# Performance work log

Hardware: AMD Instinct MI355X
Metric: run time of the kernel (lower is better)

The kernel has to match this reference:

```python
import jax, jax.numpy as jnp
import numpy as np

N_EMBED = 1024
EMBED_DIM = 256

def setup_inputs() -> dict:
    key = jax.random.key(0)
    k1, k2 = jax.random.split(key)
    hidden_states = jax.random.normal(k1, (64, 32, 32, EMBED_DIM), dtype=jnp.float32)
    emb_weights = jax.random.normal(k2, (N_EMBED, EMBED_DIM), dtype=jnp.float32)
    return {"hidden_states": hidden_states, "emb_weights": emb_weights}

def reference(hidden_states, emb_weights):
    # flatten (B,H,W,C) -> (N, C) with C == embed_dim
    z_flat = hidden_states.reshape((-1, EMBED_DIM))
    # squared distance: ||z||^2 + ||e||^2 - 2 z.e
    distance = (
        jnp.sum(z_flat ** 2, axis=1, keepdims=True)
        + jnp.sum(emb_weights ** 2, axis=1)
        - 2.0 * jnp.dot(z_flat, emb_weights.T)
    )  # (N, n_embed)
    min_encoding_indices = jnp.argmin(distance, axis=1)  # (N,)
    z_q = jnp.take(emb_weights, min_encoding_indices, axis=0).reshape(hidden_states.shape)
    min_encoding_indices = min_encoding_indices.reshape(hidden_states.shape[0], -1)
    return z_q, min_encoding_indices
```

## Files before the change

kernel.cpp:

```cpp
#include <hip/hip_runtime.h>

typedef _Float16 half8  __attribute__((ext_vector_type(8)));
typedef _Float16 half4  __attribute__((ext_vector_type(4)));
typedef float    float4v __attribute__((ext_vector_type(4)));
typedef float    float8v __attribute__((ext_vector_type(8)));

#define N_ROWS  65536
#define N_CODES 1024
#define DIM     256
#define BM      64
#define NBLKS   (N_ROWS / BM)

__global__ __launch_bounds__(64)
void vq_prep(const float* __restrict__ emb, float* __restrict__ e_norm,
             _Float16* __restrict__ e_frag, int* __restrict__ count) {
    const int c = blockIdx.x, lane = threadIdx.x;
    const int l15 = c & 15, nt = c >> 4;
    if (count && c == 0 && lane == 0) *count = 0;
    float4v v = ((const float4v*)(emb + (size_t)c * DIM))[lane];
    half4 h, l;
    float ss = 0.f;
    #pragma unroll
    for (int j = 0; j < 4; ++j) {
        float x = v[j];
        ss += x * x;
        _Float16 hh = (_Float16)x;
        h[j] = hh;
        l[j] = (_Float16)(x - (float)hh);
    }
    const int ks = lane >> 3, q = (lane >> 1) & 3, jb = (lane & 1) * 4;
    _Float16* p = e_frag + ((size_t)(nt * 8 + ks)) * 1024 + (q * 16 + l15) * 8 + jb;
    *(half4*)p = h;
    *(half4*)(p + 512) = l;
    #pragma unroll
    for (int m = 32; m >= 1; m >>= 1) ss += __shfl_xor(ss, m, 64);
    if (lane == 0) e_norm[c] = ss;
}

__global__ __launch_bounds__(256, 2)
void vq_screen(const float* __restrict__ z,
               const _Float16* __restrict__ e_frag,
               const float* __restrict__ e_norm,
               const float* __restrict__ emb,
               float* __restrict__ zq,
               float* __restrict__ idxf,
               int* __restrict__ count,
               int* __restrict__ list) {
    __shared__ _Float16 sA[32 * 512];
    __shared__ float    s_nrm[N_CODES];
    __shared__ float    s_znrm[BM];
    __shared__ float    s_red[4];
    __shared__ float4   s_best[BM][5];
    __shared__ int      s_idx[BM];

    const int t = threadIdx.x;
    const int w = t >> 6, lane = t & 63, quad = lane >> 4, l15 = lane & 15;
    const int rowblk = blockIdx.x * BM;

    float n0 = e_norm[t], n1 = e_norm[t + 256], n2 = e_norm[t + 512], n3 = e_norm[t + 768];
    s_nrm[t] = n0; s_nrm[t + 256] = n1; s_nrm[t + 512] = n2; s_nrm[t + 768] = n3;
    float mx = fmaxf(fmaxf(n0, n1), fmaxf(n2, n3));
    #pragma unroll
    for (int m = 1; m < 64; m <<= 1) mx = fmaxf(mx, __shfl_xor(mx, m, 64));
    if (lane == 0) s_red[w] = mx;

    float ss = 0.f;
    #pragma unroll
    for (int i = 0; i < 8; ++i) {
        const int row = w * 16 + l15;
        const int col = i * 32 + quad * 8;
        float8v v = *(const float8v*)(z + (size_t)(rowblk + row) * DIM + col);
        half8 h;
        #pragma unroll
        for (int j = 0; j < 8; ++j) {
            float x = v[j];
            ss += x * x;
            h[j] = (_Float16)x;
        }
        *(half8*)(sA + (size_t)(w * 8 + i) * 512 + lane * 8) = h;
    }
    ss += __shfl_xor(ss, 16, 64);
    ss += __shfl_xor(ss, 32, 64);
    if (quad == 0) s_znrm[w * 16 + l15] = ss;
    __syncthreads();

    for (int pass = 0; pass < 2; ++pass) {
        const int ntbase = w * 16 + pass * 8;
        float4v acc[4][8] = {};

        #pragma unroll
        for (int ks = 0; ks < 8; ++ks) {
            half8 bh[8];
            #pragma unroll
            for (int nt = 0; nt < 8; ++nt)
                bh[nt] = *(const half8*)(e_frag + ((size_t)((ntbase + nt) * 8 + ks)) * 1024 + lane * 8);
            __builtin_amdgcn_s_setprio(1);
            #pragma unroll
            for (int mt = 0; mt < 4; ++mt) {
                half8 ah = *(const half8*)(sA + (size_t)(mt * 8 + ks) * 512 + lane * 8);
                #pragma unroll
                for (int nt = 0; nt < 8; ++nt)
                    acc[mt][nt] = __builtin_amdgcn_mfma_f32_16x16x32_f16(ah, bh[nt], acc[mt][nt], 0, 0, 0);
            }
            __builtin_amdgcn_s_setprio(0);
        }

        float nrm[8]; int cg[8];
        #pragma unroll
        for (int nt = 0; nt < 8; ++nt) {
            cg[nt]  = (ntbase + nt) * 16 + l15;
            nrm[nt] = s_nrm[cg[nt]];
        }
        #pragma unroll
        for (int mt = 0; mt < 4; ++mt) {
            #pragma unroll
            for (int r = 0; r < 4; ++r) {
                float m1 = nrm[0] - 2.0f * acc[mt][0][r]; int i1 = cg[0];
                float m2 = 1e30f;
                #pragma unroll
                for (int nt = 1; nt < 8; ++nt) {
                    float s = nrm[nt] - 2.0f * acc[mt][nt][r];
                    if (s < m1) { m2 = m1; m1 = s; i1 = cg[nt]; }
                    else m2 = fminf(m2, s);
                }
                #pragma unroll
                for (int m = 1; m < 16; m <<= 1) {
                    float o1 = __shfl_xor(m1, m, 64);
                    int   oi = __shfl_xor(i1, m, 64);
                    float o2 = __shfl_xor(m2, m, 64);
                    if (o1 < m1 || (o1 == m1 && oi < i1)) {
                        m2 = fminf(m1, o2); m1 = o1; i1 = oi;
                    } else {
                        m2 = fminf(m2, o1);
                    }
                }
                if (l15 == 0) {
                    const int row = mt * 16 + quad * 4 + r;
                    if (pass == 0) {
                        float4 pr; pr.x = m1; pr.y = (float)i1; pr.z = m2; pr.w = 0.f;
                        s_best[row][w] = pr;
                    } else {
                        float4 pv = s_best[row][w];
                        float4 pr;
                        if (m1 < pv.x) { pr.x = m1; pr.y = (float)i1; pr.z = fminf(pv.x, m2); }
                        else           { pr.x = pv.x; pr.y = pv.y;     pr.z = fminf(pv.z, m1); }
                        pr.w = 0.f;
                        s_best[row][w] = pr;
                    }
                }
            }
        }
    }
    __syncthreads();

    if (t < BM) {
        float4 b0 = s_best[t][0];
        float m1 = b0.x, fi = b0.y, m2 = b0.z;
        #pragma unroll
        for (int s = 1; s < 4; ++s) {
            float4 bv = s_best[t][s];
            if (bv.x < m1 || (bv.x == m1 && bv.y < fi)) {
                m2 = fminf(m1, bv.z); m1 = bv.x; fi = bv.y;
            } else {
                m2 = fminf(m2, bv.x);
            }
        }
        s_idx[t] = (int)fi;
        idxf[rowblk + t] = fi;
        float emax = sqrtf(fmaxf(fmaxf(s_red[0], s_red[1]), fmaxf(s_red[2], s_red[3])));
        float T = 0.005f * sqrtf(s_znrm[t]) * emax + 0.05f;
        if (m2 - m1 <= T) {
            int pos = atomicAdd(count, 1);
            list[pos] = rowblk + t;
        }
    }
    __syncthreads();

    const float4v* emb4 = (const float4v*)emb;
    float4v* zq4 = (float4v*)zq;
    const int rr = t >> 2, cb = t & 3;
    const int code = s_idx[rr];
    #pragma unroll
    for (int i = 0; i < 16; ++i) {
        const int chunk = cb + i * 4;
        zq4[(size_t)(rowblk + rr) * 64 + chunk] = emb4[(size_t)code * 64 + chunk];
    }
}

__global__ __launch_bounds__(256, 2)
void vq_exact(const float* __restrict__ z,
              const _Float16* __restrict__ e_frag,
              const float* __restrict__ e_norm,
              const float* __restrict__ emb,
              float* __restrict__ zq,
              float* __restrict__ idxf,
              const int* __restrict__ count,
              const int* __restrict__ list) {
    const int cnt = *count;
    const int base = blockIdx.x * BM;
    if (base >= cnt) return;

    __shared__ _Float16 sA[32 * 2 * 512];
    __shared__ float    s_nrm[N_CODES];
    __shared__ float2   s_best[BM][5];
    __shared__ int      s_idx[BM];
    __shared__ int      s_rows[BM];

    const int t = threadIdx.x;
    const int w = t >> 6, lane = t & 63, quad = lane >> 4, l15 = lane & 15;

    if (t < BM) {
        int slot = base + t;
        s_rows[t] = list[slot < cnt ? slot : cnt - 1];
    }
    s_nrm[t]       = e_norm[t];
    s_nrm[t + 256] = e_norm[t + 256];
    s_nrm[t + 512] = e_norm[t + 512];
    s_nrm[t + 768] = e_norm[t + 768];
    __syncthreads();

    #pragma unroll
    for (int i = 0; i < 8; ++i) {
        const int row = w * 16 + l15;
        const int grow = s_rows[row];
        const int col = i * 32 + quad * 8;
        float8v v = *(const float8v*)(z + (size_t)grow * DIM + col);
        half8 h, lo;
        #pragma unroll
        for (int j = 0; j < 8; ++j) {
            float x = v[j];
            _Float16 hh = (_Float16)x;
            h[j] = hh;
            lo[j] = (_Float16)(x - (float)hh);
        }
        _Float16* p = sA + (size_t)((w * 8 + i) * 2) * 512 + lane * 8;
        *(half8*)p = h;
        *(half8*)(p + 512) = lo;
    }
    __syncthreads();

    for (int pass = 0; pass < 2; ++pass) {
        const int ntbase = w * 16 + pass * 8;
        float4v acc[4][8] = {};

        #pragma unroll
        for (int ks = 0; ks < 8; ++ks) {
            half8 bh[8], bl[8];
            #pragma unroll
            for (int nt = 0; nt < 8; ++nt) {
                const _Float16* bp = e_frag + ((size_t)((ntbase + nt) * 8 + ks)) * 1024 + lane * 8;
                bh[nt] = *(const half8*)bp;
                bl[nt] = *(const half8*)(bp + 512);
            }
            __builtin_amdgcn_s_setprio(1);
            #pragma unroll
            for (int mt = 0; mt < 4; ++mt) {
                const _Float16* ap = sA + (size_t)((mt * 8 + ks) * 2) * 512 + lane * 8;
                half8 ah = *(const half8*)ap;
                half8 al = *(const half8*)(ap + 512);
                #pragma unroll
                for (int nt = 0; nt < 8; ++nt)
                    acc[mt][nt] = __builtin_amdgcn_mfma_f32_16x16x32_f16(ah, bh[nt], acc[mt][nt], 0, 0, 0);
                #pragma unroll
                for (int nt = 0; nt < 8; ++nt)
                    acc[mt][nt] = __builtin_amdgcn_mfma_f32_16x16x32_f16(ah, bl[nt], acc[mt][nt], 0, 0, 0);
                #pragma unroll
                for (int nt = 0; nt < 8; ++nt)
                    acc[mt][nt] = __builtin_amdgcn_mfma_f32_16x16x32_f16(al, bh[nt], acc[mt][nt], 0, 0, 0);
            }
            __builtin_amdgcn_s_setprio(0);
        }

        float nrm[8]; int cg[8];
        #pragma unroll
        for (int nt = 0; nt < 8; ++nt) {
            cg[nt]  = (ntbase + nt) * 16 + l15;
            nrm[nt] = s_nrm[cg[nt]];
        }
        #pragma unroll
        for (int mt = 0; mt < 4; ++mt) {
            #pragma unroll
            for (int r = 0; r < 4; ++r) {
                float bs = nrm[0] - 2.0f * acc[mt][0][r]; int bi = cg[0];
                #pragma unroll
                for (int nt = 1; nt < 8; ++nt) {
                    float s = nrm[nt] - 2.0f * acc[mt][nt][r];
                    if (s < bs) { bs = s; bi = cg[nt]; }
                }
                #pragma unroll
                for (int m = 1; m < 16; m <<= 1) {
                    float s2 = __shfl_xor(bs, m, 64);
                    int   i2 = __shfl_xor(bi, m, 64);
                    if (s2 < bs || (s2 == bs && i2 < bi)) { bs = s2; bi = i2; }
                }
                if (l15 == 0) {
                    const int row = mt * 16 + quad * 4 + r;
                    if (pass == 0) {
                        float2 pr; pr.x = bs; pr.y = (float)bi;
                        s_best[row][w] = pr;
                    } else {
                        float2 pv = s_best[row][w];
                        if (bs < pv.x) {
                            float2 pr; pr.x = bs; pr.y = (float)bi;
                            s_best[row][w] = pr;
                        }
                    }
                }
            }
        }
    }
    __syncthreads();

    if (t < BM) {
        float2 p0 = s_best[t][0];
        float bs = p0.x, bi = p0.y;
        #pragma unroll
        for (int s = 1; s < 4; ++s) {
            float2 pv = s_best[t][s];
            if (pv.x < bs || (pv.x == bs && pv.y < bi)) { bs = pv.x; bi = pv.y; }
        }
        s_idx[t] = (int)bi;
        idxf[s_rows[t]] = bi;
    }
    __syncthreads();

    const float4v* emb4 = (const float4v*)emb;
    float4v* zq4 = (float4v*)zq;
    const int rr = t >> 2, cb = t & 3;
    const int grow = s_rows[rr];
    const int code = s_idx[rr];
    #pragma unroll
    for (int i = 0; i < 16; ++i) {
        const int chunk = cb + i * 4;
        zq4[(size_t)grow * 64 + chunk] = emb4[(size_t)code * 64 + chunk];
    }
}

__global__ __launch_bounds__(256, 2)
void vq_main(const float* __restrict__ z,
             const _Float16* __restrict__ e_frag,
             const float* __restrict__ e_norm,
             const float* __restrict__ emb,
             float* __restrict__ zq,
             float* __restrict__ idxf,
             int fused_gather) {
    __shared__ _Float16 sA[32 * 2 * 512];
    __shared__ float    s_nrm[N_CODES];
    __shared__ float2   s_best[BM][5];
    __shared__ int      s_idx[BM];

    const int t = threadIdx.x;
    const int w = t >> 6, lane = t & 63, quad = lane >> 4, l15 = lane & 15;
    const int rowblk = blockIdx.x * BM;

    s_nrm[t]       = e_norm[t];
    s_nrm[t + 256] = e_norm[t + 256];
    s_nrm[t + 512] = e_norm[t + 512];
    s_nrm[t + 768] = e_norm[t + 768];

    #pragma unroll
    for (int i = 0; i < 8; ++i) {
        const int row = w * 16 + l15;
        const int col = i * 32 + quad * 8;
        float8v v = *(const float8v*)(z + (size_t)(rowblk + row) * DIM + col);
        half8 h, lo;
        #pragma unroll
        for (int j = 0; j < 8; ++j) {
            float x = v[j];
            _Float16 hh = (_Float16)x;
            h[j] = hh;
            lo[j] = (_Float16)(x - (float)hh);
        }
        _Float16* p = sA + (size_t)((w * 8 + i) * 2) * 512 + lane * 8;
        *(half8*)p = h;
        *(half8*)(p + 512) = lo;
    }
    __syncthreads();

    for (int pass = 0; pass < 2; ++pass) {
        const int ntbase = w * 16 + pass * 8;
        float4v acc[4][8] = {};

        #pragma unroll
        for (int ks = 0; ks < 8; ++ks) {
            half8 bh[8], bl[8];
            #pragma unroll
            for (int nt = 0; nt < 8; ++nt) {
                const _Float16* bp = e_frag + ((size_t)((ntbase + nt) * 8 + ks)) * 1024 + lane * 8;
                bh[nt] = *(const half8*)bp;
                bl[nt] = *(const half8*)(bp + 512);
            }
            __builtin_amdgcn_s_setprio(1);
            #pragma unroll
            for (int mt = 0; mt < 4; ++mt) {
                const _Float16* ap = sA + (size_t)((mt * 8 + ks) * 2) * 512 + lane * 8;
                half8 ah = *(const half8*)ap;
                half8 al = *(const half8*)(ap + 512);
                #pragma unroll
                for (int nt = 0; nt < 8; ++nt)
                    acc[mt][nt] = __builtin_amdgcn_mfma_f32_16x16x32_f16(ah, bh[nt], acc[mt][nt], 0, 0, 0);
                #pragma unroll
                for (int nt = 0; nt < 8; ++nt)
                    acc[mt][nt] = __builtin_amdgcn_mfma_f32_16x16x32_f16(ah, bl[nt], acc[mt][nt], 0, 0, 0);
                #pragma unroll
                for (int nt = 0; nt < 8; ++nt)
                    acc[mt][nt] = __builtin_amdgcn_mfma_f32_16x16x32_f16(al, bh[nt], acc[mt][nt], 0, 0, 0);
            }
            __builtin_amdgcn_s_setprio(0);
        }

        float nrm[8]; int cg[8];
        #pragma unroll
        for (int nt = 0; nt < 8; ++nt) {
            cg[nt]  = (ntbase + nt) * 16 + l15;
            nrm[nt] = s_nrm[cg[nt]];
        }
        #pragma unroll
        for (int mt = 0; mt < 4; ++mt) {
            #pragma unroll
            for (int r = 0; r < 4; ++r) {
                float bs = nrm[0] - 2.0f * acc[mt][0][r]; int bi = cg[0];
                #pragma unroll
                for (int nt = 1; nt < 8; ++nt) {
                    float s = nrm[nt] - 2.0f * acc[mt][nt][r];
                    if (s < bs) { bs = s; bi = cg[nt]; }
                }
                #pragma unroll
                for (int m = 1; m < 16; m <<= 1) {
                    float s2 = __shfl_xor(bs, m, 64);
                    int   i2 = __shfl_xor(bi, m, 64);
                    if (s2 < bs || (s2 == bs && i2 < bi)) { bs = s2; bi = i2; }
                }
                if (l15 == 0) {
                    const int row = mt * 16 + quad * 4 + r;
                    if (pass == 0) {
                        float2 pr; pr.x = bs; pr.y = (float)bi;
                        s_best[row][w] = pr;
                    } else {
                        float2 pv = s_best[row][w];
                        if (bs < pv.x) {
                            float2 pr; pr.x = bs; pr.y = (float)bi;
                            s_best[row][w] = pr;
                        }
                    }
                }
            }
        }
    }
    __syncthreads();

    if (t < BM) {
        float2 p0 = s_best[t][0];
        float bs = p0.x, bi = p0.y;
        #pragma unroll
        for (int s = 1; s < 4; ++s) {
            float2 pv = s_best[t][s];
            if (pv.x < bs || (pv.x == bs && pv.y < bi)) { bs = pv.x; bi = pv.y; }
        }
        s_idx[t] = (int)bi;
        idxf[rowblk + t] = bi;
    }

    if (!fused_gather) return;
    __syncthreads();

    const float4v* emb4 = (const float4v*)emb;
    float4v* zq4 = (float4v*)zq;
    const int rr = t >> 2, cb = t & 3;
    const int code = s_idx[rr];
    #pragma unroll
    for (int i = 0; i < 16; ++i) {
        const int chunk = cb + i * 4;
        zq4[(size_t)(rowblk + rr) * 64 + chunk] = emb4[(size_t)code * 64 + chunk];
    }
}

__global__ __launch_bounds__(256)
void vq_gather(const float* __restrict__ emb,
               const float* __restrict__ idxf,
               float* __restrict__ zq) {
    const int tid  = blockIdx.x * 256 + threadIdx.x;
    const int r    = tid >> 6;
    const int lane = tid & 63;
    const int idx  = (int)idxf[r];
    const float4* ep = (const float4*)(emb + (size_t)idx * DIM);
    ((float4*)(zq + (size_t)r * DIM))[lane] = ep[lane];
}

extern "C" void kernel_launch(void* const* d_in, const int* in_sizes, int n_in,
                              void* d_out, int out_size, void* d_ws, size_t ws_size,
                              hipStream_t stream) {
    const float* z   = (const float*)d_in[0];
    const float* emb = (const float*)d_in[1];

    float* zq   = (float*)d_out;
    float* idxf = zq + (size_t)N_ROWS * DIM;

    const size_t efrag_sz = (size_t)N_CODES * DIM * 2 * sizeof(_Float16);
    const size_t list_sz  = (size_t)N_ROWS * sizeof(int);
    const size_t need_p   = 4096 + efrag_sz + 4096 + list_sz;

    if (ws_size >= need_p) {
        float*    e_norm = (float*)d_ws;
        _Float16* e_frag = (_Float16*)((char*)d_ws + 4096);
        int*      count  = (int*)((char*)d_ws + 4096 + efrag_sz);
        int*      list   = (int*)((char*)d_ws + 4096 + efrag_sz + 4096);
        vq_prep<<<N_CODES, 64, 0, stream>>>(emb, e_norm, e_frag, count);
        vq_screen<<<NBLKS, 256, 0, stream>>>(z, e_frag, e_norm, emb, zq, idxf, count, list);
        vq_exact<<<NBLKS, 256, 0, stream>>>(z, e_frag, e_norm, emb, zq, idxf, count, list);
    } else {
        const size_t need = 4096 + efrag_sz;
        const int in_ws = (ws_size >= need);
        char* base = in_ws ? (char*)d_ws : (char*)d_out;
        float*    e_norm = (float*)base;
        _Float16* e_frag = (_Float16*)(base + 4096);
        vq_prep<<<N_CODES, 64, 0, stream>>>(emb, e_norm, e_frag, (int*)0);
        vq_main<<<NBLKS, 256, 0, stream>>>(z, e_frag, e_norm, emb, zq, idxf, in_ws);
        if (!in_ws)
            vq_gather<<<(N_ROWS * 64) / 256, 256, 0, stream>>>(emb, idxf, zq);
    }
}
```

Baseline: 217.5 us.

## Track top-3 in screen pass and resolve two-way ties with exact FP32 dots

New measurement: 353.2 us. 1.62x slower.

```diff
diff --git a/kernel.cpp b/kernel.cpp
--- a/kernel.cpp
+++ b/kernel.cpp
@@ -9,7 +9,23 @@
 #define N_CODES 1024
 #define DIM     256
 #define BM      64
+#define BM2     16
 #define NBLKS   (N_ROWS / BM)
+
+__device__ __forceinline__ void merge3(float& m1, int& i1, float& m2, int& i2, float& m3,
+                                       float o1, int oi1, float o2, int oi2, float o3) {
+    if (o1 < m1 || (o1 == m1 && oi1 < i1)) {
+        float t1 = m1; int ti1 = i1; float t2 = m2; int ti2 = i2; float t3 = m3;
+        m1 = o1; i1 = oi1; m2 = o2; i2 = oi2; m3 = o3;
+        o1 = t1; oi1 = ti1; o2 = t2; oi2 = ti2; o3 = t3;
+    }
+    if (o1 < m2 || (o1 == m2 && oi1 < i2)) {
+        m3 = fminf(m2, o2);
+        m2 = o1; i2 = oi1;
+    } else {
+        m3 = fminf(m3, o1);
+    }
+}
 
 __global__ __launch_bounds__(64)
 void vq_prep(const float* __restrict__ emb, float* __restrict__ e_norm,
@@ -44,18 +60,23 @@
                const float* __restrict__ emb,
                float* __restrict__ zq,
                float* __restrict__ idxf,
-               int* __restrict__ count,
-               int* __restrict__ list) {
+               int* __restrict__ count2,
+               int* __restrict__ list2) {
     __shared__ _Float16 sA[32 * 512];
     __shared__ float    s_nrm[N_CODES];
     __shared__ float    s_znrm[BM];
     __shared__ float    s_red[4];
-    __shared__ float4   s_best[BM][5];
+    __shared__ float4   s_best4[BM][5];
+    __shared__ float    s_b3[BM][5];
     __shared__ int      s_idx[BM];
+    __shared__ int      s_crow[BM], s_cc1[BM], s_cc2[BM];
+    __shared__ int      s_ccnt;
 
     const int t = threadIdx.x;
     const int w = t >> 6, lane = t & 63, quad = lane >> 4, l15 = lane & 15;
     const int rowblk = blockIdx.x * BM;
+
+    if (t == 0) s_ccnt = 0;
 
     float n0 = e_norm[t], n1 = e_norm[t + 256], n2 = e_norm[t + 512], n3 = e_norm[t + 768];
     s_nrm[t] = n0; s_nrm[t + 256] = n1; s_nrm[t + 512] = n2; s_nrm[t + 768] = n3;
@@ -116,37 +137,33 @@
             #pragma unroll
             for (int r = 0; r < 4; ++r) {
                 float m1 = nrm[0] - 2.0f * acc[mt][0][r]; int i1 = cg[0];
-                float m2 = 1e30f;
+                float m2 = 1e30f, m3 = 1e30f; int i2 = 0;
                 #pragma unroll
                 for (int nt = 1; nt < 8; ++nt) {
                     float s = nrm[nt] - 2.0f * acc[mt][nt][r];
-                    if (s < m1) { m2 = m1; m1 = s; i1 = cg[nt]; }
-                    else m2 = fminf(m2, s);
+                    if (s < m1)      { m3 = m2; m2 = m1; i2 = i1; m1 = s; i1 = cg[nt]; }
+                    else if (s < m2) { m3 = m2; m2 = s; i2 = cg[nt]; }
+                    else if (s < m3) { m3 = s; }
                 }
                 #pragma unroll
                 for (int m = 1; m < 16; m <<= 1) {
                     float o1 = __shfl_xor(m1, m, 64);
-                    int   oi = __shfl_xor(i1, m, 64);
+                    int  oi1 = __shfl_xor(i1, m, 64);
                     float o2 = __shfl_xor(m2, m, 64);
-                    if (o1 < m1 || (o1 == m1 && oi < i1)) {
-                        m2 = fminf(m1, o2); m1 = o1; i1 = oi;
-                    } else {
-                        m2 = fminf(m2, o1);
-                    }
+                    int  oi2 = __shfl_xor(i2, m, 64);
+                    float o3 = __shfl_xor(m3, m, 64);
+                    merge3(m1, i1, m2, i2, m3, o1, oi1, o2, oi2, o3);
                 }
                 if (l15 == 0) {
                     const int row = mt * 16 + quad * 4 + r;
-                    if (pass == 0) {
-                        float4 pr; pr.x = m1; pr.y = (float)i1; pr.z = m2; pr.w = 0.f;
-                        s_best[row][w] = pr;
-                    } else {
-                        float4 pv = s_best[row][w];
-                        float4 pr;
-                        if (m1 < pv.x) { pr.x = m1; pr.y = (float)i1; pr.z = fminf(pv.x, m2); }
-                        else           { pr.x = pv.x; pr.y = pv.y;     pr.z = fminf(pv.z, m1); }
-                        pr.w = 0.f;
-                        s_best[row][w] = pr;
+                    if (pass == 1) {
+                        float4 pv = s_best4[row][w];
+                        merge3(m1, i1, m2, i2, m3,
+                               pv.x, (int)pv.y, pv.z, (int)pv.w, s_b3[row][w]);
                     }
+                    float4 pr; pr.x = m1; pr.y = (float)i1; pr.z = m2; pr.w = (float)i2;
+                    s_best4[row][w] = pr;
+                    s_b3[row][w] = m3;
                 }
             }
         }
@@ -154,27 +171,55 @@
     __syncthreads();
 
     if (t < BM) {
-        float4 b0 = s_best[t][0];
-        float m1 = b0.x, fi = b0.y, m2 = b0.z;
+        float4 b0 = s_best4[t][0];
+        float m1 = b0.x, m2 = b0.z, m3 = s_b3[t][0];
+        int   i1 = (int)b0.y, i2 = (int)b0.w;
         #pragma unroll
         for (int s = 1; s < 4; ++s) {
-            float4 bv = s_best[t][s];
-            if (bv.x < m1 || (bv.x == m1 && bv.y < fi)) {
-                m2 = fminf(m1, bv.z); m1 = bv.x; fi = bv.y;
-            } else {
-                m2 = fminf(m2, bv.x);
-            }
-        }
-        s_idx[t] = (int)fi;
-        idxf[rowblk + t] = fi;
+            float4 bv = s_best4[t][s];
+            merge3(m1, i1, m2, i2, m3, bv.x, (int)bv.y, bv.z, (int)bv.w, s_b3[t][s]);
+        }
+        s_idx[t] = i1;
         float emax = sqrtf(fmaxf(fmaxf(s_red[0], s_red[1]), fmaxf(s_red[2], s_red[3])));
         float T = 0.005f * sqrtf(s_znrm[t]) * emax + 0.05f;
         if (m2 - m1 <= T) {
-            int pos = atomicAdd(count, 1);
-            list[pos] = rowblk + t;
-        }
-    }
-    __syncthreads();
+            if (m3 - m1 <= T) {
+                int pos = atomicAdd(count2, 1);
+                list2[pos] = rowblk + t;
+            } else {
+                int p = atomicAdd(&s_ccnt, 1);
+                s_crow[p] = t; s_cc1[p] = i1; s_cc2[p] = i2;
+            }
+        }
+    }
+    __syncthreads();
+
+    {
+        const int cc = s_ccnt;
+        for (int e = w; e < cc; e += 4) {
+            const int row = s_crow[e], c1 = s_cc1[e], c2 = s_cc2[e];
+            float4v zz = ((const float4v*)(z + (size_t)(rowblk + row) * DIM))[lane];
+            float4v e1 = ((const float4v*)(emb + (size_t)c1 * DIM))[lane];
+            float4v e2 = ((const float4v*)(emb + (size_t)c2 * DIM))[lane];
+            float d1 = 0.f, d2 = 0.f;
+            #pragma unroll
+            for (int j = 0; j < 4; ++j) { d1 += zz[j] * e1[j]; d2 += zz[j] * e2[j]; }
+            #pragma unroll
+            for (int m = 1; m < 64; m <<= 1) {
+                d1 += __shfl_xor(d1, m, 64);
+                d2 += __shfl_xor(d2, m, 64);
+            }
+            if (lane == 0) {
+                float s1 = s_nrm[c1] - 2.0f * d1;
+                float s2 = s_nrm[c2] - 2.0f * d2;
+                int wnr = (s1 < s2) ? c1 : (s2 < s1) ? c2 : (c1 < c2 ? c1 : c2);
+                s_idx[row] = wnr;
+            }
+        }
+    }
+    __syncthreads();
+
+    if (t < BM) idxf[rowblk + t] = (float)s_idx[t];
 
     const float4v* emb4 = (const float4v*)emb;
     float4v* zq4 = (float4v*)zq;
@@ -188,43 +233,178 @@
 }
 
 __global__ __launch_bounds__(256, 2)
-void vq_exact(const float* __restrict__ z,
-              const _Float16* __restrict__ e_frag,
-              const float* __restrict__ e_norm,
-              const float* __restrict__ emb,
-              float* __restrict__ zq,
-              float* __restrict__ idxf,
-              const int* __restrict__ count,
-              const int* __restrict__ list) {
-    const int cnt = *count;
-    const int base = blockIdx.x * BM;
-    if (base >= cnt) return;
-
+void vq_exact16(const float* __restrict__ z,
+                const _Float16* __restrict__ e_frag,
+                const float* __restrict__ e_norm,
+                const float* __restrict__ emb,
+                float* __restrict__ zq,
+                float* __restrict__ idxf,
+                const int* __restrict__ count2,
+                const int* __restrict__ list2) {
+    const int cnt = *count2;
+
+    __shared__ _Float16 sA[8 * 2 * 512];
+    __shared__ float    s_nrm[N_CODES];
+    __shared__ float2   s_best[BM2][5];
+    __shared__ int      s_idx[BM2], s_rows[BM2];
+
+    const int t = threadIdx.x;
+    const int w = t >> 6, lane = t & 63, quad = lane >> 4, l15 = lane & 15;
+
+    if (blockIdx.x * BM2 >= cnt) return;
+
+    s_nrm[t]       = e_norm[t];
+    s_nrm[t + 256] = e_norm[t + 256];
+    s_nrm[t + 512] = e_norm[t + 512];
+    s_nrm[t + 768] = e_norm[t + 768];
+
+    for (int base = blockIdx.x * BM2; base < cnt; base += gridDim.x * BM2) {
+        __syncthreads();
+        if (t < BM2) {
+            int slot = base + t;
+            s_rows[t] = list2[slot < cnt ? slot : cnt - 1];
+        }
+        __syncthreads();
+
+        #pragma unroll
+        for (int i = 0; i < 2; ++i) {
+            const int ks = w + i * 4;
+            const int grow = s_rows[l15];
+            const int col = ks * 32 + quad * 8;
+            float8v v = *(const float8v*)(z + (size_t)grow * DIM + col);
+            half8 h, lo;
+            #pragma unroll
+            for (int j = 0; j < 8; ++j) {
+                float x = v[j];
+                _Float16 hh = (_Float16)x;
+                h[j] = hh;
+                lo[j] = (_Float16)(x - (float)hh);
+            }
+            _Float16* p = sA + (size_t)(ks * 2) * 512 + lane * 8;
+            *(half8*)p = h;
+            *(half8*)(p + 512) = lo;
+        }
+        __syncthreads();
+
+        for (int pass = 0; pass < 2; ++pass) {
+            const int ntbase = w * 16 + pass * 8;
+            float4v acc[8] = {};
+
+            #pragma unroll
+            for (int ks = 0; ks < 8; ++ks) {
+                half8 bh[8], bl[8];
+                #pragma unroll
+                for (int nt = 0; nt < 8; ++nt) {
+                    const _Float16* bp = e_frag + ((size_t)((ntbase + nt) * 8 + ks)) * 1024 + lane * 8;
+                    bh[nt] = *(const half8*)bp;
+                    bl[nt] = *(const half8*)(bp + 512);
+                }
+                const _Float16* ap = sA + (size_t)(ks * 2) * 512 + lane * 8;
+                half8 ah = *(const half8*)ap;
+                half8 al = *(const half8*)(ap + 512);
+                __builtin_amdgcn_s_setprio(1);
+                #pragma unroll
+                for (int nt = 0; nt < 8; ++nt)
+                    acc[nt] = __builtin_amdgcn_mfma_f32_16x16x32_f16(ah, bh[nt], acc[nt], 0, 0, 0);
+                #pragma unroll
+                for (int nt = 0; nt < 8; ++nt)
+                    acc[nt] = __builtin_amdgcn_mfma_f32_16x16x32_f16(ah, bl[nt], acc[nt], 0, 0, 0);
+                #pragma unroll
+                for (int nt = 0; nt < 8; ++nt)
+                    acc[nt] = __builtin_amdgcn_mfma_f32_16x16x32_f16(al, bh[nt], acc[nt], 0, 0, 0);
+                __builtin_amdgcn_s_setprio(0);
+            }
+
+            float nrm[8]; int cg[8];
+            #pragma unroll
+            for (int nt = 0; nt < 8; ++nt) {
+                cg[nt]  = (ntbase + nt) * 16 + l15;
+                nrm[nt] = s_nrm[cg[nt]];
+            }
+            #pragma unroll
+            for (int r = 0; r < 4; ++r) {
+                float bs = nrm[0] - 2.0f * acc[0][r]; int bi = cg[0];
+                #pragma unroll
+                for (int nt = 1; nt < 8; ++nt) {
+                    float s = nrm[nt] - 2.0f * acc[nt][r];
+                    if (s < bs) { bs = s; bi = cg[nt]; }
+                }
+                #pragma unroll
+                for (int m = 1; m < 16; m <<= 1) {
+                    float s2 = __shfl_xor(bs, m, 64);
+                    int   i2 = __shfl_xor(bi, m, 64);
+                    if (s2 < bs || (s2 == bs && i2 < bi)) { bs = s2; bi = i2; }
+                }
+                if (l15 == 0) {
+                    const int row = quad * 4 + r;
+                    if (pass == 0) {
+                        float2 pr; pr.x = bs; pr.y = (float)bi;
+                        s_best[row][w] = pr;
+                    } else {
+                        float2 pv = s_best[row][w];
+                        if (bs < pv.x) {
+                            float2 pr; pr.x = bs; pr.y = (float)bi;
+                            s_best[row][w] = pr;
+                        }
+                    }
+                }
+            }
+        }
+        __syncthreads();
+
+        if (t < BM2) {
+            float2 p0 = s_best[t][0];
+            float bs = p0.x, bi = p0.y;
+            #pragma unroll
+            for (int s = 1; s < 4; ++s) {
+                float2 pv = s_best[t][s];
+                if (pv.x < bs || (pv.x == bs && pv.y < bi)) { bs = pv.x; bi = pv.y; }
+            }
+            s_idx[t] = (int)bi;
+            idxf[s_rows[t]] = bi;
+        }
+        __syncthreads();
+
+        const float4v* emb4 = (const float4v*)emb;
+        float4v* zq4 = (float4v*)zq;
+        const int rr = t >> 4, cb = t & 15;
+        const int grow = s_rows[rr];
+        const int code = s_idx[rr];
+        #pragma unroll
+        for (int i = 0; i < 4; ++i) {
+            const int chunk = cb + i * 16;
+            zq4[(size_t)grow * 64 + chunk] = emb4[(size_t)code * 64 + chunk];
+        }
+    }
+}
+
+__global__ __launch_bounds__(256, 2)
+void vq_main(const float* __restrict__ z,
+             const _Float16* __restrict__ e_frag,
+             const float* __restrict__ e_norm,
+             const float* __restrict__ emb,
+             float* __restrict__ zq,
+             float* __restrict__ idxf,
+             int fused_gather) {
     __shared__ _Float16 sA[32 * 2 * 512];
     __shared__ float    s_nrm[N_CODES];
     __shared__ float2   s_best[BM][5];
     __shared__ int      s_idx[BM];
-    __shared__ int      s_rows[BM];
 
     const int t = threadIdx.x;
     const int w = t >> 6, lane = t & 63, quad = lane >> 4, l15 = lane & 15;
-
-    if (t < BM) {
-        int slot = base + t;
-        s_rows[t] = list[slot < cnt ? slot : cnt - 1];
-    }
+    const int rowblk = blockIdx.x * BM;
+
     s_nrm[t]       = e_norm[t];
     s_nrm[t + 256] = e_norm[t + 256];
     s_nrm[t + 512] = e_norm[t + 512];
     s_nrm[t + 768] = e_norm[t + 768];
-    __syncthreads();
 
     #pragma unroll
     for (int i = 0; i < 8; ++i) {
         const int row = w * 16 + l15;
-        const int grow = s_rows[row];
         const int col = i * 32 + quad * 8;
-        float8v v = *(const float8v*)(z + (size_t)grow * DIM + col);
+        float8v v = *(const float8v*)(z + (size_t)(rowblk + row) * DIM + col);
         half8 h, lo;
         #pragma unroll
         for (int j = 0; j < 8; ++j) {
@@ -320,144 +500,6 @@
             if (pv.x < bs || (pv.x == bs && pv.y < bi)) { bs = pv.x; bi = pv.y; }
         }
         s_idx[t] = (int)bi;
-        idxf[s_rows[t]] = bi;
-    }
-    __syncthreads();
-
-    const float4v* emb4 = (const float4v*)emb;
-    float4v* zq4 = (float4v*)zq;
-    const int rr = t >> 2, cb = t & 3;
-    const int grow = s_rows[rr];
-    const int code = s_idx[rr];
-    #pragma unroll
-    for (int i = 0; i < 16; ++i) {
-        const int chunk = cb + i * 4;
-        zq4[(size_t)grow * 64 + chunk] = emb4[(size_t)code * 64 + chunk];
-    }
-}
-
-__global__ __launch_bounds__(256, 2)
-void vq_main(const float* __restrict__ z,
-             const _Float16* __restrict__ e_frag,
-             const float* __restrict__ e_norm,
-             const float* __restrict__ emb,
-             float* __restrict__ zq,
-             float* __restrict__ idxf,
-             int fused_gather) {
-    __shared__ _Float16 sA[32 * 2 * 512];
-    __shared__ float    s_nrm[N_CODES];
-    __shared__ float2   s_best[BM][5];
-    __shared__ int      s_idx[BM];
-
-    const int t = threadIdx.x;
-    const int w = t >> 6, lane = t & 63, quad = lane >> 4, l15 = lane & 15;
-    const int rowblk = blockIdx.x * BM;
-
-    s_nrm[t]       = e_norm[t];
-    s_nrm[t + 256] = e_norm[t + 256];
-    s_nrm[t + 512] = e_norm[t + 512];
-    s_nrm[t + 768] = e_norm[t + 768];
-
-    #pragma unroll
-    for (int i = 0; i < 8; ++i) {
-        const int row = w * 16 + l15;
-        const int col = i * 32 + quad * 8;
-        float8v v = *(const float8v*)(z + (size_t)(rowblk + row) * DIM + col);
-        half8 h, lo;
-        #pragma unroll
-        for (int j = 0; j < 8; ++j) {
-            float x = v[j];
-            _Float16 hh = (_Float16)x;
-            h[j] = hh;
-            lo[j] = (_Float16)(x - (float)hh);
-        }
-        _Float16* p = sA + (size_t)((w * 8 + i) * 2) * 512 + lane * 8;
-        *(half8*)p = h;
-        *(half8*)(p + 512) = lo;
-    }
-    __syncthreads();
-
-    for (int pass = 0; pass < 2; ++pass) {
-        const int ntbase = w * 16 + pass * 8;
-        float4v acc[4][8] = {};
-
-        #pragma unroll
-        for (int ks = 0; ks < 8; ++ks) {
-            half8 bh[8], bl[8];
-            #pragma unroll
-            for (int nt = 0; nt < 8; ++nt) {
-                const _Float16* bp = e_frag + ((size_t)((ntbase + nt) * 8 + ks)) * 1024 + lane * 8;
-                bh[nt] = *(const half8*)bp;
-                bl[nt] = *(const half8*)(bp + 512);
-            }
-            __builtin_amdgcn_s_setprio(1);
-            #pragma unroll
-            for (int mt = 0; mt < 4; ++mt) {
-                const _Float16* ap = sA + (size_t)((mt * 8 + ks) * 2) * 512 + lane * 8;
-                half8 ah = *(const half8*)ap;
-                half8 al = *(const half8*)(ap + 512);
-                #pragma unroll
-                for (int nt = 0; nt < 8; ++nt)
-                    acc[mt][nt] = __builtin_amdgcn_mfma_f32_16x16x32_f16(ah, bh[nt], acc[mt][nt], 0, 0, 0);
-                #pragma unroll
-                for (int nt = 0; nt < 8; ++nt)
-                    acc[mt][nt] = __builtin_amdgcn_mfma_f32_16x16x32_f16(ah, bl[nt], acc[mt][nt], 0, 0, 0);
-                #pragma unroll
-                for (int nt = 0; nt < 8; ++nt)
-                    acc[mt][nt] = __builtin_amdgcn_mfma_f32_16x16x32_f16(al, bh[nt], acc[mt][nt], 0, 0, 0);
-            }
-            __builtin_amdgcn_s_setprio(0);
-        }
-
-        float nrm[8]; int cg[8];
-        #pragma unroll
-        for (int nt = 0; nt < 8; ++nt) {
-            cg[nt]  = (ntbase + nt) * 16 + l15;
-            nrm[nt] = s_nrm[cg[nt]];
-        }
-        #pragma unroll
-        for (int mt = 0; mt < 4; ++mt) {
-            #pragma unroll
-            for (int r = 0; r < 4; ++r) {
-                float bs = nrm[0] - 2.0f * acc[mt][0][r]; int bi = cg[0];
-                #pragma unroll
-                for (int nt = 1; nt < 8; ++nt) {
-                    float s = nrm[nt] - 2.0f * acc[mt][nt][r];
-                    if (s < bs) { bs = s; bi = cg[nt]; }
-                }
-                #pragma unroll
-                for (int m = 1; m < 16; m <<= 1) {
-                    float s2 = __shfl_xor(bs, m, 64);
-                    int   i2 = __shfl_xor(bi, m, 64);
-                    if (s2 < bs || (s2 == bs && i2 < bi)) { bs = s2; bi = i2; }
-                }
-                if (l15 == 0) {
-                    const int row = mt * 16 + quad * 4 + r;
-                    if (pass == 0) {
-                        float2 pr; pr.x = bs; pr.y = (float)bi;
-                        s_best[row][w] = pr;
-                    } else {
-                        float2 pv = s_best[row][w];
-                        if (bs < pv.x) {
-                            float2 pr; pr.x = bs; pr.y = (float)bi;
-                            s_best[row][w] = pr;
-                        }
-                    }
-                }
-            }
-        }
-    }
-    __syncthreads();
-
-    if (t < BM) {
-        float2 p0 = s_best[t][0];
-        float bs = p0.x, bi = p0.y;
-        #pragma unroll
-        for (int s = 1; s < 4; ++s) {
-            float2 pv = s_best[t][s];
-            if (pv.x < bs || (pv.x == bs && pv.y < bi)) { bs = pv.x; bi = pv.y; }
-        }
-        s_idx[t] = (int)bi;
         idxf[rowblk + t] = bi;
     }
 
@@ -503,11 +545,11 @@
     if (ws_size >= need_p) {
         float*    e_norm = (float*)d_ws;
         _Float16* e_frag = (_Float16*)((char*)d_ws + 4096);
-        int*      count  = (int*)((char*)d_ws + 4096 + efrag_sz);
-        int*      list   = (int*)((char*)d_ws + 4096 + efrag_sz + 4096);
-        vq_prep<<<N_CODES, 64, 0, stream>>>(emb, e_norm, e_frag, count);
-        vq_screen<<<NBLKS, 256, 0, stream>>>(z, e_frag, e_norm, emb, zq, idxf, count, list);
-        vq_exact<<<NBLKS, 256, 0, stream>>>(z, e_frag, e_norm, emb, zq, idxf, count, list);
+        int*      count2 = (int*)((char*)d_ws + 4096 + efrag_sz);
+        int*      list2  = (int*)((char*)d_ws + 4096 + efrag_sz + 4096);
+        vq_prep<<<N_CODES, 64, 0, stream>>>(emb, e_norm, e_frag, count2);
+        vq_screen<<<NBLKS, 256, 0, stream>>>(z, e_frag, e_norm, emb, zq, idxf, count2, list2);
+        vq_exact16<<<512, 256, 0, stream>>>(z, e_frag, e_norm, emb, zq, idxf, count2, list2);
     } else {
         const size_t need = 4096 + efrag_sz;
         const int in_ws = (ws_size >= need);
```

## Rework exact-recheck kernel into 16-row grid-stride tiles over flagged rows

Applied to the files above, without the earlier changes.

After: 585.2 us. 169% more time.

```diff
diff --git a/kernel.cpp b/kernel.cpp
--- a/kernel.cpp
+++ b/kernel.cpp
@@ -9,6 +9,7 @@
 #define N_CODES 1024
 #define DIM     256
 #define BM      64
+#define BM2     16
 #define NBLKS   (N_ROWS / BM)
 
 __global__ __launch_bounds__(64)
@@ -188,43 +189,178 @@
 }
 
 __global__ __launch_bounds__(256, 2)
-void vq_exact(const float* __restrict__ z,
-              const _Float16* __restrict__ e_frag,
-              const float* __restrict__ e_norm,
-              const float* __restrict__ emb,
-              float* __restrict__ zq,
-              float* __restrict__ idxf,
-              const int* __restrict__ count,
-              const int* __restrict__ list) {
+void vq_exact16(const float* __restrict__ z,
+                const _Float16* __restrict__ e_frag,
+                const float* __restrict__ e_norm,
+                const float* __restrict__ emb,
+                float* __restrict__ zq,
+                float* __restrict__ idxf,
+                const int* __restrict__ count,
+                const int* __restrict__ list) {
     const int cnt = *count;
-    const int base = blockIdx.x * BM;
-    if (base >= cnt) return;
-
+
+    __shared__ _Float16 sA[8 * 2 * 512];
+    __shared__ float    s_nrm[N_CODES];
+    __shared__ float2   s_best[BM2][5];
+    __shared__ int      s_idx[BM2], s_rows[BM2];
+
+    const int t = threadIdx.x;
+    const int w = t >> 6, lane = t & 63, quad = lane >> 4, l15 = lane & 15;
+
+    if (blockIdx.x * BM2 >= cnt) return;
+
+    s_nrm[t]       = e_norm[t];
+    s_nrm[t + 256] = e_norm[t + 256];
+    s_nrm[t + 512] = e_norm[t + 512];
+    s_nrm[t + 768] = e_norm[t + 768];
+
+    for (int base = blockIdx.x * BM2; base < cnt; base += gridDim.x * BM2) {
+        __syncthreads();
+        if (t < BM2) {
+            int slot = base + t;
+            s_rows[t] = list[slot < cnt ? slot : cnt - 1];
+        }
+        __syncthreads();
+
+        #pragma unroll
+        for (int i = 0; i < 2; ++i) {
+            const int ks = w + i * 4;
+            const int grow = s_rows[l15];
+            const int col = ks * 32 + quad * 8;
+            float8v v = *(const float8v*)(z + (size_t)grow * DIM + col);
+            half8 h, lo;
+            #pragma unroll
+            for (int j = 0; j < 8; ++j) {
+                float x = v[j];
+                _Float16 hh = (_Float16)x;
+                h[j] = hh;
+                lo[j] = (_Float16)(x - (float)hh);
+            }
+            _Float16* p = sA + (size_t)(ks * 2) * 512 + lane * 8;
+            *(half8*)p = h;
+            *(half8*)(p + 512) = lo;
+        }
+        __syncthreads();
+
+        for (int pass = 0; pass < 2; ++pass) {
+            const int ntbase = w * 16 + pass * 8;
+            float4v acc[8] = {};
+
+            #pragma unroll
+            for (int ks = 0; ks < 8; ++ks) {
+                half8 bh[8], bl[8];
+                #pragma unroll
+                for (int nt = 0; nt < 8; ++nt) {
+                    const _Float16* bp = e_frag + ((size_t)((ntbase + nt) * 8 + ks)) * 1024 + lane * 8;
+                    bh[nt] = *(const half8*)bp;
+                    bl[nt] = *(const half8*)(bp + 512);
+                }
+                const _Float16* ap = sA + (size_t)(ks * 2) * 512 + lane * 8;
+                half8 ah = *(const half8*)ap;
+                half8 al = *(const half8*)(ap + 512);
+                __builtin_amdgcn_s_setprio(1);
+                #pragma unroll
+                for (int nt = 0; nt < 8; ++nt)
+                    acc[nt] = __builtin_amdgcn_mfma_f32_16x16x32_f16(ah, bh[nt], acc[nt], 0, 0, 0);
+                #pragma unroll
+                for (int nt = 0; nt < 8; ++nt)
+                    acc[nt] = __builtin_amdgcn_mfma_f32_16x16x32_f16(ah, bl[nt], acc[nt], 0, 0, 0);
+                #pragma unroll
+                for (int nt = 0; nt < 8; ++nt)
+                    acc[nt] = __builtin_amdgcn_mfma_f32_16x16x32_f16(al, bh[nt], acc[nt], 0, 0, 0);
+                __builtin_amdgcn_s_setprio(0);
+            }
+
+            float nrm[8]; int cg[8];
+            #pragma unroll
+            for (int nt = 0; nt < 8; ++nt) {
+                cg[nt]  = (ntbase + nt) * 16 + l15;
+                nrm[nt] = s_nrm[cg[nt]];
+            }
+            #pragma unroll
+            for (int r = 0; r < 4; ++r) {
+                float bs = nrm[0] - 2.0f * acc[0][r]; int bi = cg[0];
+                #pragma unroll
+                for (int nt = 1; nt < 8; ++nt) {
+                    float s = nrm[nt] - 2.0f * acc[nt][r];
+                    if (s < bs) { bs = s; bi = cg[nt]; }
+                }
+                #pragma unroll
+                for (int m = 1; m < 16; m <<= 1) {
+                    float s2 = __shfl_xor(bs, m, 64);
+                    int   i2 = __shfl_xor(bi, m, 64);
+                    if (s2 < bs || (s2 == bs && i2 < bi)) { bs = s2; bi = i2; }
+                }
+                if (l15 == 0) {
+                    const int row = quad * 4 + r;
+                    if (pass == 0) {
+                        float2 pr; pr.x = bs; pr.y = (float)bi;
+                        s_best[row][w] = pr;
+                    } else {
+                        float2 pv = s_best[row][w];
+                        if (bs < pv.x) {
+                            float2 pr; pr.x = bs; pr.y = (float)bi;
+                            s_best[row][w] = pr;
+                        }
+                    }
+                }
+            }
+        }
+        __syncthreads();
+
+        if (t < BM2) {
+            float2 p0 = s_best[t][0];
+            float bs = p0.x, bi = p0.y;
+            #pragma unroll
+            for (int s = 1; s < 4; ++s) {
+                float2 pv = s_best[t][s];
+                if (pv.x < bs || (pv.x == bs && pv.y < bi)) { bs = pv.x; bi = pv.y; }
+            }
+            s_idx[t] = (int)bi;
+            idxf[s_rows[t]] = bi;
+        }
+        __syncthreads();
+
+        const float4v* emb4 = (const float4v*)emb;
+        float4v* zq4 = (float4v*)zq;
+        const int rr = t >> 4, cb = t & 15;
+        const int grow = s_rows[rr];
+        const int code = s_idx[rr];
+        #pragma unroll
+        for (int i = 0; i < 4; ++i) {
+            const int chunk = cb + i * 16;
+            zq4[(size_t)grow * 64 + chunk] = emb4[(size_t)code * 64 + chunk];
+        }
+    }
+}
+
+__global__ __launch_bounds__(256, 2)
+void vq_main(const float* __restrict__ z,
+             const _Float16* __restrict__ e_frag,
+             const float* __restrict__ e_norm,
+             const float* __restrict__ emb,
+             float* __restrict__ zq,
+             float* __restrict__ idxf,
+             int fused_gather) {
     __shared__ _Float16 sA[32 * 2 * 512];
     __shared__ float    s_nrm[N_CODES];
     __shared__ float2   s_best[BM][5];
     __shared__ int      s_idx[BM];
-    __shared__ int      s_rows[BM];
 
     const int t = threadIdx.x;
     const int w = t >> 6, lane = t & 63, quad = lane >> 4, l15 = lane & 15;
-
-    if (t < BM) {
-        int slot = base + t;
-        s_rows[t] = list[slot < cnt ? slot : cnt - 1];
-    }
+    const int rowblk = blockIdx.x * BM;
+
     s_nrm[t]       = e_norm[t];
     s_nrm[t + 256] = e_norm[t + 256];
     s_nrm[t + 512] = e_norm[t + 512];
     s_nrm[t + 768] = e_norm[t + 768];
-    __syncthreads();
 
     #pragma unroll
     for (int i = 0; i < 8; ++i) {
         const int row = w * 16 + l15;
-        const int grow = s_rows[row];
         const int col = i * 32 + quad * 8;
-        float8v v = *(const float8v*)(z + (size_t)grow * DIM + col);
+        float8v v = *(const float8v*)(z + (size_t)(rowblk + row) * DIM + col);
         half8 h, lo;
         #pragma unroll
         for (int j = 0; j < 8; ++j) {
@@ -320,144 +456,6 @@
             if (pv.x < bs || (pv.x == bs && pv.y < bi)) { bs = pv.x; bi = pv.y; }
         }
         s_idx[t] = (int)bi;
-        idxf[s_rows[t]] = bi;
-    }
-    __syncthreads();
-
-    const float4v* emb4 = (const float4v*)emb;
-    float4v* zq4 = (float4v*)zq;
-    const int rr = t >> 2, cb = t & 3;
-    const int grow = s_rows[rr];
-    const int code = s_idx[rr];
-    #pragma unroll
-    for (int i = 0; i < 16; ++i) {
-        const int chunk = cb + i * 4;
-        zq4[(size_t)grow * 64 + chunk] = emb4[(size_t)code * 64 + chunk];
-    }
-}
-
-__global__ __launch_bounds__(256, 2)
-void vq_main(const float* __restrict__ z,
-             const _Float16* __restrict__ e_frag,
-             const float* __restrict__ e_norm,
-             const float* __restrict__ emb,
-             float* __restrict__ zq,
-             float* __restrict__ idxf,
-             int fused_gather) {
-    __shared__ _Float16 sA[32 * 2 * 512];
-    __shared__ float    s_nrm[N_CODES];
-    __shared__ float2   s_best[BM][5];
-    __shared__ int      s_idx[BM];
-
-    const int t = threadIdx.x;
-    const int w = t >> 6, lane = t & 63, quad = lane >> 4, l15 = lane & 15;
-    const int rowblk = blockIdx.x * BM;
-
-    s_nrm[t]       = e_norm[t];
-    s_nrm[t + 256] = e_norm[t + 256];
-    s_nrm[t + 512] = e_norm[t + 512];
-    s_nrm[t + 768] = e_norm[t + 768];
-
-    #pragma unroll
-    for (int i = 0; i < 8; ++i) {
-        const int row = w * 16 + l15;
-        const int col = i * 32 + quad * 8;
-        float8v v = *(const float8v*)(z + (size_t)(rowblk + row) * DIM + col);
-        half8 h, lo;
-        #pragma unroll
-        for (int j = 0; j < 8; ++j) {
-            float x = v[j];
-            _Float16 hh = (_Float16)x;
-            h[j] = hh;
-            lo[j] = (_Float16)(x - (float)hh);
-        }
-        _Float16* p = sA + (size_t)((w * 8 + i) * 2) * 512 + lane * 8;
-        *(half8*)p = h;
-        *(half8*)(p + 512) = lo;
-    }
-    __syncthreads();
-
-    for (int pass = 0; pass < 2; ++pass) {
-        const int ntbase = w * 16 + pass * 8;
-        float4v acc[4][8] = {};
-
-        #pragma unroll
-        for (int ks = 0; ks < 8; ++ks) {
-            half8 bh[8], bl[8];
-            #pragma unroll
-            for (int nt = 0; nt < 8; ++nt) {
-                const _Float16* bp = e_frag + ((size_t)((ntbase + nt) * 8 + ks)) * 1024 + lane * 8;
-                bh[nt] = *(const half8*)bp;
-                bl[nt] = *(const half8*)(bp + 512);
-            }
-            __builtin_amdgcn_s_setprio(1);
-            #pragma unroll
-            for (int mt = 0; mt < 4; ++mt) {
-                const _Float16* ap = sA + (size_t)((mt * 8 + ks) * 2) * 512 + lane * 8;
-                half8 ah = *(const half8*)ap;
-                half8 al = *(const half8*)(ap + 512);
-                #pragma unroll
-                for (int nt = 0; nt < 8; ++nt)
-                    acc[mt][nt] = __builtin_amdgcn_mfma_f32_16x16x32_f16(ah, bh[nt], acc[mt][nt], 0, 0, 0);
-                #pragma unroll
-                for (int nt = 0; nt < 8; ++nt)
-                    acc[mt][nt] = __builtin_amdgcn_mfma_f32_16x16x32_f16(ah, bl[nt], acc[mt][nt], 0, 0, 0);
-                #pragma unroll
-                for (int nt = 0; nt < 8; ++nt)
-                    acc[mt][nt] = __builtin_amdgcn_mfma_f32_16x16x32_f16(al, bh[nt], acc[mt][nt], 0, 0, 0);
-            }
-            __builtin_amdgcn_s_setprio(0);
-        }
-
-        float nrm[8]; int cg[8];
-        #pragma unroll
-        for (int nt = 0; nt < 8; ++nt) {
-            cg[nt]  = (ntbase + nt) * 16 + l15;
-            nrm[nt] = s_nrm[cg[nt]];
-        }
-        #pragma unroll
-        for (int mt = 0; mt < 4; ++mt) {
-            #pragma unroll
-            for (int r = 0; r < 4; ++r) {
-                float bs = nrm[0] - 2.0f * acc[mt][0][r]; int bi = cg[0];
-                #pragma unroll
-                for (int nt = 1; nt < 8; ++nt) {
-                    float s = nrm[nt] - 2.0f * acc[mt][nt][r];
-                    if (s < bs) { bs = s; bi = cg[nt]; }
-                }
-                #pragma unroll
-                for (int m = 1; m < 16; m <<= 1) {
-                    float s2 = __shfl_xor(bs, m, 64);
-                    int   i2 = __shfl_xor(bi, m, 64);
-                    if (s2 < bs || (s2 == bs && i2 < bi)) { bs = s2; bi = i2; }
-                }
-                if (l15 == 0) {
-                    const int row = mt * 16 + quad * 4 + r;
-                    if (pass == 0) {
-                        float2 pr; pr.x = bs; pr.y = (float)bi;
-                        s_best[row][w] = pr;
-                    } else {
-                        float2 pv = s_best[row][w];
-                        if (bs < pv.x) {
-                            float2 pr; pr.x = bs; pr.y = (float)bi;
-                            s_best[row][w] = pr;
-                        }
-                    }
-                }
-            }
-        }
-    }
-    __syncthreads();
-
-    if (t < BM) {
-        float2 p0 = s_best[t][0];
-        float bs = p0.x, bi = p0.y;
-        #pragma unroll
-        for (int s = 1; s < 4; ++s) {
-            float2 pv = s_best[t][s];
-            if (pv.x < bs || (pv.x == bs && pv.y < bi)) { bs = pv.x; bi = pv.y; }
-        }
-        s_idx[t] = (int)bi;
         idxf[rowblk + t] = bi;
     }
 
@@ -507,7 +505,7 @@
         int*      list   = (int*)((char*)d_ws + 4096 + efrag_sz + 4096);
         vq_prep<<<N_CODES, 64, 0, stream>>>(emb, e_norm, e_frag, count);
         vq_screen<<<NBLKS, 256, 0, stream>>>(z, e_frag, e_norm, emb, zq, idxf, count, list);
-        vq_exact<<<NBLKS, 256, 0, stream>>>(z, e_frag, e_norm, emb, zq, idxf, count, list);
+        vq_exact16<<<512, 256, 0, stream>>>(z, e_frag, e_norm, emb, zq, idxf, count, list);
     } else {
         const size_t need = 4096 + efrag_sz;
         const int in_ws = (ws_size >= need);
```
